# Optimization experiments

Measured on AMD Instinct MI355X. Metric: run time of the kernel, lower is better.

Reference implementation:

```python
import jax, jax.numpy as jnp
import numpy as np

B, LQ, C = 4, 4096, 384
NH, NL, NP = 6, 1, 4
HL, WL = 64, 64
LV = HL * WL
DH = C // NH
EPS = 1e-6


def layer_norm(x, g, b):
    mu = jnp.mean(x, axis=-1, keepdims=True)
    var = jnp.mean(jnp.square(x - mu), axis=-1, keepdims=True)
    return (x - mu) * jax.lax.rsqrt(var + EPS) * g + b


def ms_deform_attn_core(value, spatial_shapes, level_start_index, loc, attn_w):
    # value [B,LV,NH,DH]; loc [B,LQ,NH,NL,NP,2] in [0,1]; attn_w [B,LQ,NH,NL,NP]
    ss = np.asarray(spatial_shapes)
    lsi = np.asarray(level_start_index)
    Bv, _, nH, dh = value.shape
    Lq = loc.shape[1]
    nP = loc.shape[4]
    out = jnp.zeros((Bv, Lq, nH, dh), value.dtype)
    for l in range(loc.shape[3]):
        Hl, Wl = int(ss[l, 0]), int(ss[l, 1])
        st = int(lsi[l])
        vflat = value[:, st:st + Hl * Wl]  # [B, Hl*Wl, nH, dh]
        xy = loc[:, :, :, l]               # [B,LQ,nH,NP,2]
        # grid_sample(align_corners=False): pixel = loc * size - 0.5
        x = xy[..., 0] * Wl - 0.5
        y = xy[..., 1] * Hl - 0.5
        x0 = jnp.floor(x)
        y0 = jnp.floor(y)
        wx = x - x0
        wy = y - y0
        x0i = x0.astype(jnp.int32)
        y0i = y0.astype(jnp.int32)

        def gather(xi, yi):
            # zero padding outside the feature map (padding_mode='zeros')
            valid = (xi >= 0) & (xi < Wl) & (yi >= 0) & (yi < Hl)
            idx = jnp.clip(yi, 0, Hl - 1) * Wl + jnp.clip(xi, 0, Wl - 1)  # [B,LQ,nH,NP]
            idx2 = idx.transpose(0, 1, 3, 2).reshape(Bv, Lq * nP, nH)
            g = jnp.take_along_axis(vflat, idx2[..., None], axis=1)       # [B,LQ*NP,nH,dh]
            g = g.reshape(Bv, Lq, nP, nH, dh).transpose(0, 1, 3, 2, 4)    # [B,LQ,nH,NP,dh]
            return g * valid[..., None].astype(value.dtype)

        samp = (gather(x0i, y0i) * ((1 - wx) * (1 - wy))[..., None]
                + gather(x0i + 1, y0i) * (wx * (1 - wy))[..., None]
                + gather(x0i, y0i + 1) * ((1 - wx) * wy)[..., None]
                + gather(x0i + 1, y0i + 1) * (wx * wy)[..., None])
        out = out + jnp.einsum('bqhpd,bqhp->bqhd', samp, attn_w[:, :, :, l])
    return out.reshape(Bv, Lq, nH * dh)


def setup_inputs() -> dict:
    key = jax.random.key(0)
    ks = jax.random.split(key, 12)
    s = 0.02
    return {
        'query': jax.random.normal(ks[0], (B, LQ, C), jnp.float32),
        'reference_points': jax.random.uniform(ks[1], (B, LQ, NL, 2), dtype=jnp.float32),
        'feat': jax.random.normal(ks[2], (B, LV, C), jnp.float32),
        'spatial_shapes': jnp.array([[HL, WL]], jnp.int32),
        'level_start_index': jnp.array([0], jnp.int32),
        'ln_q_g': jnp.ones((C,), jnp.float32), 'ln_q_b': jnp.zeros((C,), jnp.float32),
        'ln_f_g': jnp.ones((C,), jnp.float32), 'ln_f_b': jnp.zeros((C,), jnp.float32),
        'gamma': jax.random.normal(ks[3], (C,), jnp.float32) * 0.1,
        'Wv': jax.random.normal(ks[4], (C, C), jnp.float32) * s,
        'bv': jnp.zeros((C,), jnp.float32),
        'Wo': jax.random.normal(ks[5], (C, NH * NL * NP * 2), jnp.float32) * s,
        'bo': jax.random.normal(ks[6], (NH * NL * NP * 2,), jnp.float32) * 0.5,
        'Wa': jax.random.normal(ks[7], (C, NH * NL * NP), jnp.float32) * s,
        'ba': jnp.zeros((NH * NL * NP,), jnp.float32),
        'Wout': jax.random.normal(ks[8], (C, C), jnp.float32) * s,
        'bout': jnp.zeros((C,), jnp.float32),
    }


def reference(query, reference_points, feat, spatial_shapes, level_start_index,
              ln_q_g, ln_q_b, ln_f_g, ln_f_b, gamma,
              Wv, bv, Wo, bo, Wa, ba, Wout, bout):
    q = layer_norm(query, ln_q_g, ln_q_b)
    f = layer_norm(feat, ln_f_g, ln_f_b)
    value = (f @ Wv + bv).reshape(B, LV, NH, DH)
    offsets = (q @ Wo + bo).reshape(B, LQ, NH, NL, NP, 2)
    attn_w = jax.nn.softmax((q @ Wa + ba).reshape(B, LQ, NH, NL * NP), axis=-1)
    attn_w = attn_w.reshape(B, LQ, NH, NL, NP)
    # offset normalizer is (W, H) per level
    norm = jnp.stack([spatial_shapes[:, 1], spatial_shapes[:, 0]], -1).astype(jnp.float32)
    loc = reference_points[:, :, None, :, None, :] + offsets / norm[None, None, None, :, None, :]
    attn = ms_deform_attn_core(value, spatial_shapes, level_start_index, loc, attn_w)
    attn = attn @ Wout + bout
    return query + gamma * attn
```

## Files before the change

kernel.cpp:

```cpp
#include <hip/hip_runtime.h>
#include <math.h>

#define B_    4
#define LQ_   4096
#define C_    384
#define NH_   6
#define NP_   4
#define HL_   64
#define WL_   64
#define LV_   (HL_ * WL_)
#define ROWS_ (B_ * LQ_)
#define EPS_  1e-6f
#define NOFF_ 48
#define NLOG_ 24

typedef unsigned short u16;
typedef unsigned int   u32;
typedef __bf16 bf16x8 __attribute__((ext_vector_type(8)));
typedef float  f32x4  __attribute__((ext_vector_type(4)));

__device__ __forceinline__ u16 f2bf(float f) {
    u32 u = __float_as_uint(f);
    u += 0x7fff + ((u >> 16) & 1);
    return (u16)(u >> 16);
}
__device__ __forceinline__ u32 pack2bf(float a, float b) {
    return (u32)f2bf(a) | ((u32)f2bf(b) << 16);
}

__device__ __forceinline__ f32x4 mfma16(bf16x8 a, bf16x8 b, f32x4 c) {
    return __builtin_amdgcn_mfma_f32_16x16x32_bf16(a, b, c, 0, 0, 0);
}

__device__ __forceinline__ void gl_lds16(const u16* g, u16* l) {
    __builtin_amdgcn_global_load_lds(
        (const __attribute__((address_space(1))) unsigned int*)g,
        (__attribute__((address_space(3))) unsigned int*)l, 16, 0, 0);
}

#define LN_BLOCKS_   8192
#define PREP_BLOCKS_ 1273

__global__ __launch_bounds__(256) void ln_prep(
    const float* __restrict__ query, const float* __restrict__ feat,
    const float* __restrict__ qg, const float* __restrict__ qbv,
    const float* __restrict__ fg, const float* __restrict__ fbv,
    u16* __restrict__ qout, u16* __restrict__ fout,
    const float* __restrict__ Wv, const float* __restrict__ Wout,
    const float* __restrict__ Wo, const float* __restrict__ Wa,
    const float* __restrict__ bo, const float* __restrict__ ba,
    u16* __restrict__ WvT, u16* __restrict__ WoutT, u16* __restrict__ WcT,
    float* __restrict__ bias_c)
{
    if (blockIdx.x < LN_BLOCKS_) {
        int wid  = threadIdx.x >> 6;
        int lane = threadIdx.x & 63;
        int row  = blockIdx.x * 4 + wid;
        const float *src, *g, *bsh;
        u16* dst;
        int r;
        if (row < ROWS_) { src = query; g = qg; bsh = qbv; dst = qout; r = row; }
        else             { src = feat;  g = fg; bsh = fbv; dst = fout; r = row - ROWS_; }

        const float* x = src + (size_t)r * C_;
        float4 a4 = *(const float4*)(x + 4 * lane);
        float2 a2 = *(const float2*)(x + 256 + 2 * lane);
        float v0 = a4.x, v1 = a4.y, v2 = a4.z, v3 = a4.w, v4 = a2.x, v5 = a2.y;

        float s = v0 + v1 + v2 + v3 + v4 + v5;
#pragma unroll
        for (int off = 32; off; off >>= 1) s += __shfl_xor(s, off);
        float mu = s * (1.f / C_);

        float d0 = v0 - mu, d1 = v1 - mu, d2 = v2 - mu;
        float d3 = v3 - mu, d4 = v4 - mu, d5 = v5 - mu;
        float s2 = d0*d0 + d1*d1 + d2*d2 + d3*d3 + d4*d4 + d5*d5;
#pragma unroll
        for (int off = 32; off; off >>= 1) s2 += __shfl_xor(s2, off);
        float rs = rsqrtf(s2 * (1.f / C_) + EPS_);

        float4 g4 = *(const float4*)(g + 4 * lane);
        float4 b4 = *(const float4*)(bsh + 4 * lane);
        float2 g2 = *(const float2*)(g + 256 + 2 * lane);
        float2 b2 = *(const float2*)(bsh + 256 + 2 * lane);

        float o0 = d0 * rs * g4.x + b4.x;
        float o1 = d1 * rs * g4.y + b4.y;
        float o2 = d2 * rs * g4.z + b4.z;
        float o3 = d3 * rs * g4.w + b4.w;
        float o4 = d4 * rs * g2.x + b2.x;
        float o5 = d5 * rs * g2.y + b2.y;

        u16* y = dst + (size_t)r * C_;
        uint2 w0; w0.x = pack2bf(o0, o1); w0.y = pack2bf(o2, o3);
        *(uint2*)(y + 4 * lane) = w0;
        *(u32*)(y + 256 + 2 * lane) = pack2bf(o4, o5);
    } else {
        const int KN = 384 * 384;
        int idx = (blockIdx.x - LN_BLOCKS_) * 256 + threadIdx.x;
        if (idx < KN) {
            int n = idx / 384, k = idx - n * 384;
            WvT[idx] = f2bf(Wv[k * 384 + n]);
        } else if (idx < 2 * KN) {
            int t = idx - KN;
            int n = t / 384, k = t - n * 384;
            WoutT[t] = f2bf(Wout[k * 384 + n]);
        } else if (idx < 2 * KN + 80 * 384) {
            int t = idx - 2 * KN;
            int n = t / 384, k = t - n * 384;
            float v = (n < 48) ? Wo[k * 48 + n] : (n < 72 ? Wa[k * 24 + (n - 48)] : 0.f);
            WcT[t] = f2bf(v);
        } else if (idx < 2 * KN + 80 * 384 + 80) {
            int n = idx - (2 * KN + 80 * 384);
            bias_c[n] = (n < 48) ? bo[n] : (n < 72 ? ba[n - 48] : 0.f);
        }
    }
}

__global__ __launch_bounds__(256) void gemm_combined(
    const u16* __restrict__ fb, const u16* __restrict__ qb,
    const u16* __restrict__ WvT, const u16* __restrict__ WcT,
    const float* __restrict__ bv, const float* __restrict__ bias_c,
    u16* __restrict__ valb, float* __restrict__ offs, float* __restrict__ logits)
{
    const int K = 384;
    __shared__ __align__(16) u16 As[128 * 32];
    __shared__ __align__(16) u16 Bs[128 * 32];

    int g    = blockIdx.x;
    int tid  = threadIdx.x;
    int lane = tid & 63, wid = tid >> 6;
    int fr = lane & 15, quad = lane >> 4;

    int srow = tid >> 2;
    int scol = (tid & 3) * 8;

    if (g < 384) {
        int m0 = (g & 127) * 128, n0 = (g >> 7) * 128;
        const u16* agp0 = fb  + (size_t)(m0 + srow) * K + scol;
        const u16* agp1 = fb  + (size_t)(m0 + 64 + srow) * K + scol;
        const u16* bgp0 = WvT + (size_t)(n0 + srow) * K + scol;
        const u16* bgp1 = WvT + (size_t)(n0 + 64 + srow) * K + scol;
        u16* al0 = As + tid * 8;  u16* al1 = As + 2048 + tid * 8;
        u16* bl0 = Bs + tid * 8;  u16* bl1 = Bs + 2048 + tid * 8;

        int wm = (wid >> 1) * 64, wn = (wid & 1) * 64;

        f32x4 zero = {0.f, 0.f, 0.f, 0.f};
        f32x4 acc[4][4];
#pragma unroll
        for (int i = 0; i < 4; ++i)
#pragma unroll
            for (int j = 0; j < 4; ++j) acc[i][j] = zero;

        for (int k0 = 0; k0 < K; k0 += 32) {
            gl_lds16(agp0 + k0, al0);
            gl_lds16(agp1 + k0, al1);
            gl_lds16(bgp0 + k0, bl0);
            gl_lds16(bgp1 + k0, bl1);
            __syncthreads();
            bf16x8 af[4], bfr[4];
#pragma unroll
            for (int i = 0; i < 4; ++i)
                af[i] = *(bf16x8*)&As[(wm + i * 16 + fr) * 32 + quad * 8];
#pragma unroll
            for (int j = 0; j < 4; ++j)
                bfr[j] = *(bf16x8*)&Bs[(wn + j * 16 + fr) * 32 + quad * 8];
#pragma unroll
            for (int i = 0; i < 4; ++i)
#pragma unroll
                for (int j = 0; j < 4; ++j)
                    acc[i][j] = mfma16(af[i], bfr[j], acc[i][j]);
            __syncthreads();
        }

#pragma unroll
        for (int i = 0; i < 4; ++i) {
            int row = m0 + wm + i * 16 + quad * 4;
#pragma unroll
            for (int j = 0; j < 4; ++j) {
                int col = n0 + wn + j * 16 + fr;
                float bcol = bv[col];
#pragma unroll
                for (int r = 0; r < 4; ++r)
                    valb[(size_t)(row + r) * C_ + col] = f2bf(acc[i][j][r] + bcol);
            }
        }
    } else {
        int m0 = (g - 384) * 128;
        const u16* agp0 = qb + (size_t)(m0 + srow) * K + scol;
        const u16* agp1 = qb + (size_t)(m0 + 64 + srow) * K + scol;
        u16* al0 = As + tid * 8;  u16* al1 = As + 2048 + tid * 8;
        const u16* bgp0 = WcT + (size_t)srow * K + scol;
        const u16* bgp1 = WcT + (size_t)(64 + srow) * K + scol;
        u16* bl0 = Bs + tid * 8;
        u16* bl1 = Bs + 2048 + tid * 8;

        int wm = wid * 32;

        f32x4 zero = {0.f, 0.f, 0.f, 0.f};
        f32x4 acc[2][5];
#pragma unroll
        for (int i = 0; i < 2; ++i)
#pragma unroll
            for (int j = 0; j < 5; ++j) acc[i][j] = zero;

        for (int k0 = 0; k0 < K; k0 += 32) {
            gl_lds16(agp0 + k0, al0);
            gl_lds16(agp1 + k0, al1);
            gl_lds16(bgp0 + k0, bl0);
            if (tid < 64) gl_lds16(bgp1 + k0, bl1);
            __syncthreads();
            bf16x8 af[2], bfr[5];
#pragma unroll
            for (int i = 0; i < 2; ++i)
                af[i] = *(bf16x8*)&As[(wm + i * 16 + fr) * 32 + quad * 8];
#pragma unroll
            for (int j = 0; j < 5; ++j)
                bfr[j] = *(bf16x8*)&Bs[(j * 16 + fr) * 32 + quad * 8];
#pragma unroll
            for (int i = 0; i < 2; ++i)
#pragma unroll
                for (int j = 0; j < 5; ++j)
                    acc[i][j] = mfma16(af[i], bfr[j], acc[i][j]);
            __syncthreads();
        }

#pragma unroll
        for (int i = 0; i < 2; ++i) {
            int row = m0 + wm + i * 16 + quad * 4;
#pragma unroll
            for (int j = 0; j < 5; ++j) {
                int col = j * 16 + fr;
                if (col < 72) {
                    float bcol = bias_c[col];
#pragma unroll
                    for (int r = 0; r < 4; ++r) {
                        float v = acc[i][j][r] + bcol;
                        if (col < 48) offs[(size_t)(row + r) * NOFF_ + col] = v;
                        else          logits[(size_t)(row + r) * NLOG_ + (col - 48)] = v;
                    }
                }
            }
        }
    }
}

__global__ __launch_bounds__(384) void sampler(
    const u16*  __restrict__ value,
    const float* __restrict__ rp,
    const float* __restrict__ offs,
    const float* __restrict__ logits,
    u16* __restrict__ attn)
{
    int t = threadIdx.x;
    int g = blockIdx.x;
    int b     = (g & 7) >> 1;
    int local = ((g >> 3) << 1) | (g & 1);
    int q  = t / 48, dc = t - q * 48;
    int h  = dc >> 3;
    int col0 = dc << 3;
    int r  = b * LQ_ + local * 8 + q;

    float4 lg  = *(const float4*)(logits + (size_t)r * NLOG_ + h * 4);
    float2 rpv = *(const float2*)(rp + (size_t)r * 2);
    float4 of0 = *(const float4*)(offs + (size_t)r * NOFF_ + h * 8);
    float4 of1 = *(const float4*)(offs + (size_t)r * NOFF_ + h * 8 + 4);

    float mx = fmaxf(fmaxf(lg.x, lg.y), fmaxf(lg.z, lg.w));
    float e0 = __expf(lg.x - mx), e1 = __expf(lg.y - mx);
    float e2 = __expf(lg.z - mx), e3 = __expf(lg.w - mx);
    float rden = 1.f / (e0 + e1 + e2 + e3);
    float aws[4] = {e0 * rden, e1 * rden, e2 * rden, e3 * rden};
    float oxs[4] = {of0.x, of0.z, of1.x, of1.z};
    float oys[4] = {of0.y, of0.w, of1.y, of1.w};

    const u16* vbase = value + (size_t)b * LV_ * C_ + col0;
    float acc[8] = {0.f, 0.f, 0.f, 0.f, 0.f, 0.f, 0.f, 0.f};
#pragma unroll
    for (int p = 0; p < NP_; ++p) {
        float x = rpv.x * (float)WL_ + oxs[p] - 0.5f;
        float y = rpv.y * (float)HL_ + oys[p] - 0.5f;
        float x0f = floorf(x), y0f = floorf(y);
        float wx = x - x0f, wy = y - y0f;
        int x0 = (int)x0f, y0 = (int)y0f;
#pragma unroll
        for (int c = 0; c < 4; ++c) {
            int xi = x0 + (c & 1);
            int yi = y0 + (c >> 1);
            bool valid = (xi >= 0) && (xi < WL_) && (yi >= 0) && (yi < HL_);
            int xc = xi < 0 ? 0 : (xi > WL_ - 1 ? WL_ - 1 : xi);
            int yc = yi < 0 ? 0 : (yi > HL_ - 1 ? HL_ - 1 : yi);
            float w = ((c & 1) ? wx : 1.f - wx) * ((c >> 1) ? wy : 1.f - wy) * aws[p];
            w = valid ? w : 0.f;
            bf16x8 vv = *(const bf16x8*)(vbase + (size_t)(yc * WL_ + xc) * C_);
#pragma unroll
            for (int e = 0; e < 8; ++e) acc[e] += w * (float)vv[e];
        }
    }

    uint4 o;
    o.x = pack2bf(acc[0], acc[1]);
    o.y = pack2bf(acc[2], acc[3]);
    o.z = pack2bf(acc[4], acc[5]);
    o.w = pack2bf(acc[6], acc[7]);
    *(uint4*)(attn + (size_t)r * C_ + col0) = o;
}

__global__ __launch_bounds__(256) void out_gemm(
    const u16* __restrict__ A, const u16* __restrict__ Bt,
    const float* __restrict__ bout, const float* __restrict__ gamma,
    const float* __restrict__ query, float* __restrict__ out)
{
    const int K = 384;
    __shared__ __align__(16) u16 As[128 * 32];
    __shared__ __align__(16) u16 Bs[128 * 32];

    int g    = blockIdx.x;
    int tid  = threadIdx.x;
    int lane = tid & 63, wid = tid >> 6;
    int fr = lane & 15, quad = lane >> 4;

    int srow = tid >> 2;
    int scol = (tid & 3) * 8;

    int m0 = (g & 127) * 128, n0 = (g >> 7) * 128;
    const u16* agp0 = A  + (size_t)(m0 + srow) * K + scol;
    const u16* agp1 = A  + (size_t)(m0 + 64 + srow) * K + scol;
    const u16* bgp0 = Bt + (size_t)(n0 + srow) * K + scol;
    const u16* bgp1 = Bt + (size_t)(n0 + 64 + srow) * K + scol;
    u16* al0 = As + tid * 8;  u16* al1 = As + 2048 + tid * 8;
    u16* bl0 = Bs + tid * 8;  u16* bl1 = Bs + 2048 + tid * 8;

    int wm = (wid >> 1) * 64, wn = (wid & 1) * 64;

    f32x4 zero = {0.f, 0.f, 0.f, 0.f};
    f32x4 acc[4][4];
#pragma unroll
    for (int i = 0; i < 4; ++i)
#pragma unroll
        for (int j = 0; j < 4; ++j) acc[i][j] = zero;

    for (int k0 = 0; k0 < K; k0 += 32) {
        gl_lds16(agp0 + k0, al0);
        gl_lds16(agp1 + k0, al1);
        gl_lds16(bgp0 + k0, bl0);
        gl_lds16(bgp1 + k0, bl1);
        __syncthreads();
        bf16x8 af[4], bfr[4];
#pragma unroll
        for (int i = 0; i < 4; ++i)
            af[i] = *(bf16x8*)&As[(wm + i * 16 + fr) * 32 + quad * 8];
#pragma unroll
        for (int j = 0; j < 4; ++j)
            bfr[j] = *(bf16x8*)&Bs[(wn + j * 16 + fr) * 32 + quad * 8];
#pragma unroll
        for (int i = 0; i < 4; ++i)
#pragma unroll
            for (int j = 0; j < 4; ++j)
                acc[i][j] = mfma16(af[i], bfr[j], acc[i][j]);
        __syncthreads();
    }

#pragma unroll
    for (int i = 0; i < 4; ++i) {
        int row = m0 + wm + i * 16 + quad * 4;
#pragma unroll
        for (int j = 0; j < 4; ++j) {
            int col = n0 + wn + j * 16 + fr;
            float bc = bout[col], gm = gamma[col];
#pragma unroll
            for (int r = 0; r < 4; ++r) {
                size_t o = (size_t)(row + r) * C_ + col;
                out[o] = query[o] + gm * (acc[i][j][r] + bc);
            }
        }
    }
}

extern "C" void kernel_launch(void* const* d_in, const int* in_sizes, int n_in,
                              void* d_out, int out_size, void* d_ws, size_t ws_size,
                              hipStream_t stream)
{
    const float* query  = (const float*)d_in[0];
    const float* rp     = (const float*)d_in[1];
    const float* feat   = (const float*)d_in[2];
    const float* gamma  = (const float*)d_in[9];
    const float* Wv     = (const float*)d_in[10];
    const float* bv     = (const float*)d_in[11];
    const float* Wo     = (const float*)d_in[12];
    const float* bo     = (const float*)d_in[13];
    const float* Wa     = (const float*)d_in[14];
    const float* ba     = (const float*)d_in[15];
    const float* Wout   = (const float*)d_in[16];
    const float* bout   = (const float*)d_in[17];
    float* out = (float*)d_out;

    u16* wsu    = (u16*)d_ws;
    u16* qb     = wsu;
    u16* fb     = qb    + (size_t)ROWS_ * C_;
    u16* valb   = fb    + (size_t)ROWS_ * C_;
    u16* attnb  = valb  + (size_t)ROWS_ * C_;
    u16* WvT    = attnb + (size_t)ROWS_ * C_;
    u16* WoutT  = WvT   + 384 * 384;
    u16* WcT    = WoutT + 384 * 384;
    float* offs   = (float*)(WcT + 80 * 384);
    float* logits = offs + (size_t)ROWS_ * NOFF_;
    float* bias_c = logits + (size_t)ROWS_ * NLOG_;

    ln_prep<<<LN_BLOCKS_ + PREP_BLOCKS_, 256, 0, stream>>>(
        query, feat,
        (const float*)d_in[5], (const float*)d_in[6],
        (const float*)d_in[7], (const float*)d_in[8],
        qb, fb, Wv, Wout, Wo, Wa, bo, ba, WvT, WoutT, WcT, bias_c);

    gemm_combined<<<512, 256, 0, stream>>>(fb, qb, WvT, WcT, bv, bias_c,
                                           valb, offs, logits);

    sampler<<<2048, 384, 0, stream>>>(valb, rp, offs, logits, attnb);

    out_gemm<<<384, 256, 0, stream>>>(attnb, WoutT, bout, gamma, query, out);
}
```

Measured before the change: 170.7 us.

## Double-buffer GEMM k-tiles with swizzled LDS and retile output GEMM to 96 columns

Measured after the change: 162.2 us. 1.05x faster.

```diff
diff --git a/kernel.cpp b/kernel.cpp
--- a/kernel.cpp
+++ b/kernel.cpp
@@ -13,6 +13,7 @@
 #define EPS_  1e-6f
 #define NOFF_ 48
 #define NLOG_ 24
+#define WCTR_ 96
 
 typedef unsigned short u16;
 typedef unsigned int   u32;
@@ -38,8 +39,14 @@
         (__attribute__((address_space(3))) unsigned int*)l, 16, 0, 0);
 }
 
+__device__ __forceinline__ void vm_wait8() { asm volatile("s_waitcnt vmcnt(8)" ::: "memory"); }
+__device__ __forceinline__ void vm_wait7() { asm volatile("s_waitcnt vmcnt(7)" ::: "memory"); }
+__device__ __forceinline__ void vm_wait0() { asm volatile("s_waitcnt vmcnt(0)" ::: "memory"); }
+__device__ __forceinline__ void lgkm0()    { asm volatile("s_waitcnt lgkmcnt(0)" ::: "memory"); }
+__device__ __forceinline__ void barrier_() { asm volatile("s_barrier" ::: "memory"); }
+
 #define LN_BLOCKS_   8192
-#define PREP_BLOCKS_ 1273
+#define PREP_BLOCKS_ 1297
 
 __global__ __launch_bounds__(256) void ln_prep(
     const float* __restrict__ query, const float* __restrict__ feat,
@@ -105,13 +112,13 @@
             int t = idx - KN;
             int n = t / 384, k = t - n * 384;
             WoutT[t] = f2bf(Wout[k * 384 + n]);
-        } else if (idx < 2 * KN + 80 * 384) {
+        } else if (idx < 2 * KN + WCTR_ * 384) {
             int t = idx - 2 * KN;
             int n = t / 384, k = t - n * 384;
             float v = (n < 48) ? Wo[k * 48 + n] : (n < 72 ? Wa[k * 24 + (n - 48)] : 0.f);
             WcT[t] = f2bf(v);
-        } else if (idx < 2 * KN + 80 * 384 + 80) {
-            int n = idx - (2 * KN + 80 * 384);
+        } else if (idx < 2 * KN + WCTR_ * 384 + 80) {
+            int n = idx - (2 * KN + WCTR_ * 384);
             bias_c[n] = (n < 48) ? bo[n] : (n < 72 ? ba[n - 48] : 0.f);
         }
     }
@@ -123,26 +130,24 @@
     const float* __restrict__ bv, const float* __restrict__ bias_c,
     u16* __restrict__ valb, float* __restrict__ offs, float* __restrict__ logits)
 {
-    const int K = 384;
-    __shared__ __align__(16) u16 As[128 * 32];
-    __shared__ __align__(16) u16 Bs[128 * 32];
+    __shared__ __align__(16) u16 As_[2][8192];
+    __shared__ __align__(16) u16 Bs_[2][8192];
 
     int g    = blockIdx.x;
     int tid  = threadIdx.x;
     int lane = tid & 63, wid = tid >> 6;
     int fr = lane & 15, quad = lane >> 4;
 
-    int srow = tid >> 2;
-    int scol = (tid & 3) * 8;
+    int swz  = (fr & 7) * 8;
+    int off0 = (quad * 8) ^ swz;
+
+    int srow = tid >> 3;
+    int csw  = ((tid & 7) ^ (srow & 7)) * 8;
 
     if (g < 384) {
         int m0 = (g & 127) * 128, n0 = (g >> 7) * 128;
-        const u16* agp0 = fb  + (size_t)(m0 + srow) * K + scol;
-        const u16* agp1 = fb  + (size_t)(m0 + 64 + srow) * K + scol;
-        const u16* bgp0 = WvT + (size_t)(n0 + srow) * K + scol;
-        const u16* bgp1 = WvT + (size_t)(n0 + 64 + srow) * K + scol;
-        u16* al0 = As + tid * 8;  u16* al1 = As + 2048 + tid * 8;
-        u16* bl0 = Bs + tid * 8;  u16* bl1 = Bs + 2048 + tid * 8;
+        const u16* aSrc = fb  + (size_t)(m0 + srow) * 384 + csw;
+        const u16* bSrc = WvT + (size_t)(n0 + srow) * 384 + csw;
 
         int wm = (wid >> 1) * 64, wn = (wid & 1) * 64;
 
@@ -153,26 +158,39 @@
 #pragma unroll
             for (int j = 0; j < 4; ++j) acc[i][j] = zero;
 
-        for (int k0 = 0; k0 < K; k0 += 32) {
-            gl_lds16(agp0 + k0, al0);
-            gl_lds16(agp1 + k0, al1);
-            gl_lds16(bgp0 + k0, bl0);
-            gl_lds16(bgp1 + k0, bl1);
-            __syncthreads();
-            bf16x8 af[4], bfr[4];
+#define STGV(bu, t) { _Pragma("unroll") for (int l = 0; l < 4; ++l) { \
+            gl_lds16(aSrc + (size_t)l * (32*384) + (t)*64, &As_[bu][tid*8 + l*2048]); \
+            gl_lds16(bSrc + (size_t)l * (32*384) + (t)*64, &Bs_[bu][tid*8 + l*2048]); } }
+
+        STGV(0, 0)
+        STGV(1, 1)
+#pragma unroll
+        for (int t = 0; t < 6; ++t) {
+            const int bu = t & 1;
+            if (t < 5) vm_wait8(); else vm_wait0();
+            barrier_();
+            bf16x8 af[4][2], bfr[4][2];
+#pragma unroll
+            for (int i = 0; i < 4; ++i) {
+                int ra = (wm + i * 16 + fr) * 64;
+                af[i][0]  = *(const bf16x8*)&As_[bu][ra + off0];
+                af[i][1]  = *(const bf16x8*)&As_[bu][ra + (off0 ^ 32)];
+                int rb = (wn + i * 16 + fr) * 64;
+                bfr[i][0] = *(const bf16x8*)&Bs_[bu][rb + off0];
+                bfr[i][1] = *(const bf16x8*)&Bs_[bu][rb + (off0 ^ 32)];
+            }
+            lgkm0();
+            barrier_();
+            if (t < 4) STGV(bu, t + 2)
 #pragma unroll
             for (int i = 0; i < 4; ++i)
-                af[i] = *(bf16x8*)&As[(wm + i * 16 + fr) * 32 + quad * 8];
-#pragma unroll
-            for (int j = 0; j < 4; ++j)
-                bfr[j] = *(bf16x8*)&Bs[(wn + j * 16 + fr) * 32 + quad * 8];
-#pragma unroll
-            for (int i = 0; i < 4; ++i)
-#pragma unroll
-                for (int j = 0; j < 4; ++j)
-                    acc[i][j] = mfma16(af[i], bfr[j], acc[i][j]);
-            __syncthreads();
-        }
+#pragma unroll
+                for (int j = 0; j < 4; ++j) {
+                    acc[i][j] = mfma16(af[i][0], bfr[j][0], acc[i][j]);
+                    acc[i][j] = mfma16(af[i][1], bfr[j][1], acc[i][j]);
+                }
+        }
+#undef STGV
 
 #pragma unroll
         for (int i = 0; i < 4; ++i) {
@@ -188,13 +206,8 @@
         }
     } else {
         int m0 = (g - 384) * 128;
-        const u16* agp0 = qb + (size_t)(m0 + srow) * K + scol;
-        const u16* agp1 = qb + (size_t)(m0 + 64 + srow) * K + scol;
-        u16* al0 = As + tid * 8;  u16* al1 = As + 2048 + tid * 8;
-        const u16* bgp0 = WcT + (size_t)srow * K + scol;
-        const u16* bgp1 = WcT + (size_t)(64 + srow) * K + scol;
-        u16* bl0 = Bs + tid * 8;
-        u16* bl1 = Bs + 2048 + tid * 8;
+        const u16* aSrc = qb  + (size_t)(m0 + srow) * 384 + csw;
+        const u16* bSrc = WcT + (size_t)srow * 384 + csw;
 
         int wm = wid * 32;
 
@@ -205,26 +218,43 @@
 #pragma unroll
             for (int j = 0; j < 5; ++j) acc[i][j] = zero;
 
-        for (int k0 = 0; k0 < K; k0 += 32) {
-            gl_lds16(agp0 + k0, al0);
-            gl_lds16(agp1 + k0, al1);
-            gl_lds16(bgp0 + k0, bl0);
-            if (tid < 64) gl_lds16(bgp1 + k0, bl1);
-            __syncthreads();
-            bf16x8 af[2], bfr[5];
+#define STGS(bu, t) { _Pragma("unroll") for (int l = 0; l < 4; ++l) \
+            gl_lds16(aSrc + (size_t)l * (32*384) + (t)*64, &As_[bu][tid*8 + l*2048]); \
+            _Pragma("unroll") for (int l = 0; l < 3; ++l) \
+            gl_lds16(bSrc + (size_t)l * (32*384) + (t)*64, &Bs_[bu][tid*8 + l*2048]); }
+
+        STGS(0, 0)
+        STGS(1, 1)
+#pragma unroll
+        for (int t = 0; t < 6; ++t) {
+            const int bu = t & 1;
+            if (t < 5) vm_wait7(); else vm_wait0();
+            barrier_();
+            bf16x8 af[2][2], bfr[5][2];
+#pragma unroll
+            for (int i = 0; i < 2; ++i) {
+                int ra = (wm + i * 16 + fr) * 64;
+                af[i][0] = *(const bf16x8*)&As_[bu][ra + off0];
+                af[i][1] = *(const bf16x8*)&As_[bu][ra + (off0 ^ 32)];
+            }
+#pragma unroll
+            for (int j = 0; j < 5; ++j) {
+                int rb = (j * 16 + fr) * 64;
+                bfr[j][0] = *(const bf16x8*)&Bs_[bu][rb + off0];
+                bfr[j][1] = *(const bf16x8*)&Bs_[bu][rb + (off0 ^ 32)];
+            }
+            lgkm0();
+            barrier_();
+            if (t < 4) STGS(bu, t + 2)
 #pragma unroll
             for (int i = 0; i < 2; ++i)
-                af[i] = *(bf16x8*)&As[(wm + i * 16 + fr) * 32 + quad * 8];
-#pragma unroll
-            for (int j = 0; j < 5; ++j)
-                bfr[j] = *(bf16x8*)&Bs[(j * 16 + fr) * 32 + quad * 8];
-#pragma unroll
-            for (int i = 0; i < 2; ++i)
-#pragma unroll
-                for (int j = 0; j < 5; ++j)
-                    acc[i][j] = mfma16(af[i], bfr[j], acc[i][j]);
-            __syncthreads();
-        }
+#pragma unroll
+                for (int j = 0; j < 5; ++j) {
+                    acc[i][j] = mfma16(af[i][0], bfr[j][0], acc[i][j]);
+                    acc[i][j] = mfma16(af[i][1], bfr[j][1], acc[i][j]);
+                }
+        }
+#undef STGS
 
 #pragma unroll
         for (int i = 0; i < 2; ++i) {
@@ -312,61 +342,75 @@
     const float* __restrict__ bout, const float* __restrict__ gamma,
     const float* __restrict__ query, float* __restrict__ out)
 {
-    const int K = 384;
-    __shared__ __align__(16) u16 As[128 * 32];
-    __shared__ __align__(16) u16 Bs[128 * 32];
+    __shared__ __align__(16) u16 As_[2][8192];
+    __shared__ __align__(16) u16 Bs_[2][8192];
 
     int g    = blockIdx.x;
     int tid  = threadIdx.x;
     int lane = tid & 63, wid = tid >> 6;
     int fr = lane & 15, quad = lane >> 4;
 
-    int srow = tid >> 2;
-    int scol = (tid & 3) * 8;
-
-    int m0 = (g & 127) * 128, n0 = (g >> 7) * 128;
-    const u16* agp0 = A  + (size_t)(m0 + srow) * K + scol;
-    const u16* agp1 = A  + (size_t)(m0 + 64 + srow) * K + scol;
-    const u16* bgp0 = Bt + (size_t)(n0 + srow) * K + scol;
-    const u16* bgp1 = Bt + (size_t)(n0 + 64 + srow) * K + scol;
-    u16* al0 = As + tid * 8;  u16* al1 = As + 2048 + tid * 8;
-    u16* bl0 = Bs + tid * 8;  u16* bl1 = Bs + 2048 + tid * 8;
-
-    int wm = (wid >> 1) * 64, wn = (wid & 1) * 64;
+    int swz  = (fr & 7) * 8;
+    int off0 = (quad * 8) ^ swz;
+    int srow = tid >> 3;
+    int csw  = ((tid & 7) ^ (srow & 7)) * 8;
+
+    int m0 = (g & 127) * 128, n0 = (g >> 7) * 96;
+    const u16* aSrc = A  + (size_t)(m0 + srow) * 384 + csw;
+    const u16* bSrc = Bt + (size_t)(n0 + srow) * 384 + csw;
+
+    int wm = (wid >> 1) * 64, wn = (wid & 1) * 48;
 
     f32x4 zero = {0.f, 0.f, 0.f, 0.f};
-    f32x4 acc[4][4];
+    f32x4 acc[4][3];
 #pragma unroll
     for (int i = 0; i < 4; ++i)
 #pragma unroll
-        for (int j = 0; j < 4; ++j) acc[i][j] = zero;
-
-    for (int k0 = 0; k0 < K; k0 += 32) {
-        gl_lds16(agp0 + k0, al0);
-        gl_lds16(agp1 + k0, al1);
-        gl_lds16(bgp0 + k0, bl0);
-        gl_lds16(bgp1 + k0, bl1);
-        __syncthreads();
-        bf16x8 af[4], bfr[4];
+        for (int j = 0; j < 3; ++j) acc[i][j] = zero;
+
+#define STGO(bu, t) { _Pragma("unroll") for (int l = 0; l < 4; ++l) \
+        gl_lds16(aSrc + (size_t)l * (32*384) + (t)*64, &As_[bu][tid*8 + l*2048]); \
+        _Pragma("unroll") for (int l = 0; l < 3; ++l) \
+        gl_lds16(bSrc + (size_t)l * (32*384) + (t)*64, &Bs_[bu][tid*8 + l*2048]); }
+
+    STGO(0, 0)
+    STGO(1, 1)
+#pragma unroll
+    for (int t = 0; t < 6; ++t) {
+        const int bu = t & 1;
+        if (t < 5) vm_wait7(); else vm_wait0();
+        barrier_();
+        bf16x8 af[4][2], bfr[3][2];
+#pragma unroll
+        for (int i = 0; i < 4; ++i) {
+            int ra = (wm + i * 16 + fr) * 64;
+            af[i][0] = *(const bf16x8*)&As_[bu][ra + off0];
+            af[i][1] = *(const bf16x8*)&As_[bu][ra + (off0 ^ 32)];
+        }
+#pragma unroll
+        for (int j = 0; j < 3; ++j) {
+            int rb = (wn + j * 16 + fr) * 64;
+            bfr[j][0] = *(const bf16x8*)&Bs_[bu][rb + off0];
+            bfr[j][1] = *(const bf16x8*)&Bs_[bu][rb + (off0 ^ 32)];
+        }
+        lgkm0();
+        barrier_();
+        if (t < 4) STGO(bu, t + 2)
 #pragma unroll
         for (int i = 0; i < 4; ++i)
-            af[i] = *(bf16x8*)&As[(wm + i * 16 + fr) * 32 + quad * 8];
-#pragma unroll
-        for (int j = 0; j < 4; ++j)
-            bfr[j] = *(bf16x8*)&Bs[(wn + j * 16 + fr) * 32 + quad * 8];
-#pragma unroll
-        for (int i = 0; i < 4; ++i)
-#pragma unroll
-            for (int j = 0; j < 4; ++j)
-                acc[i][j] = mfma16(af[i], bfr[j], acc[i][j]);
-        __syncthreads();
+#pragma unroll
+            for (int j = 0; j < 3; ++j) {
+                acc[i][j] = mfma16(af[i][0], bfr[j][0], acc[i][j]);
+                acc[i][j] = mfma16(af[i][1], bfr[j][1], acc[i][j]);
+            }
     }
+#undef STGO
 
 #pragma unroll
     for (int i = 0; i < 4; ++i) {
         int row = m0 + wm + i * 16 + quad * 4;
 #pragma unroll
-        for (int j = 0; j < 4; ++j) {
+        for (int j = 0; j < 3; ++j) {
             int col = n0 + wn + j * 16 + fr;
             float bc = bout[col], gm = gamma[col];
 #pragma unroll
@@ -404,7 +448,7 @@
     u16* WvT    = attnb + (size_t)ROWS_ * C_;
     u16* WoutT  = WvT   + 384 * 384;
     u16* WcT    = WoutT + 384 * 384;
-    float* offs   = (float*)(WcT + 80 * 384);
+    float* offs   = (float*)(WcT + WCTR_ * 384);
     float* logits = offs + (size_t)ROWS_ * NOFF_;
     float* bias_c = logits + (size_t)ROWS_ * NLOG_;
 
@@ -419,5 +463,5 @@
 
     sampler<<<2048, 384, 0, stream>>>(valb, rp, offs, logits, attnb);
 
-    out_gemm<<<384, 256, 0, stream>>>(attnb, WoutT, bout, gamma, query, out);
-}
+    out_gemm<<<512, 256, 0, stream>>>(attnb, WoutT, bout, gamma, query, out);
+}
```
